# Optimization experiments

Hardware: AMD Instinct MI355X
Metric: run time of the kernel (lower is better)

Reference implementation:

```python
import jax, jax.numpy as jnp
import numpy as np


def setup_inputs() -> dict:
    key = jax.random.key(0)
    k1, k2 = jax.random.split(key)
    B, C, H, W, T = 8, 256, 64, 64, 512
    F_s = jax.random.normal(k1, (B, C, H, W), dtype=jnp.float32)
    F_t = jax.random.normal(k2, (B, T, C), dtype=jnp.float32)
    return {"F_s": F_s, "F_t": F_t}


def reference(F_s, F_t):
    B, C, H, W = F_s.shape
    T = F_t.shape[1]
    # [B, HW, C] spatial tokens
    F_s_t = jnp.transpose(F_s, (0, 2, 3, 1)).reshape(B, H * W, C)
    # scores [B, HW, T], scaled by sqrt(T) (softmax over last axis)
    A = jnp.einsum('bnc,btc->bnt', F_s_t, F_t) / jnp.sqrt(jnp.float32(T))
    A = jax.nn.softmax(A, axis=-1)
    # A^T @ F_s_t -> updated text tokens [B, T, C]
    F_t_updated = jnp.einsum('bnt,bnc->btc', A, F_s_t)
    # A @ F_t -> spatial update [B, HW, C]
    F_s_t_update = jnp.einsum('bnt,btc->bnc', A, F_t)
    F_s_t_update = jnp.transpose(F_s_t_update.reshape(B, H, W, C), (0, 3, 1, 2))
    F_s_updated = F_s + F_s_t_update
    return (F_s_updated, F_t_updated)
```

## Files before the change

kernel.cpp:

```cpp
#include <hip/hip_runtime.h>
#include <hip/hip_bf16.h>
#include <stdint.h>


typedef __attribute__((ext_vector_type(8))) short short8v;
typedef __attribute__((ext_vector_type(4))) float float4v;

#define MFMA16(a, b, c) __builtin_amdgcn_mfma_f32_16x16x32_bf16(a, b, c, 0, 0, 0)
#define SCALE 0.04419417382415922f

static __device__ __forceinline__ unsigned short f2bf(float f) {
  union { float f; uint32_t u; } v; v.f = f;
  uint32_t r = v.u + 0x7fffu + ((v.u >> 16) & 1u);
  return (unsigned short)(r >> 16);
}
static __device__ __forceinline__ float bf2f(unsigned short u) {
  union { uint32_t u; float f; } v; v.u = (uint32_t)u << 16;
  return v.f;
}

static __device__ __forceinline__ void gload16(const void* g, void* l) {
  __builtin_amdgcn_global_load_lds(
      (const __attribute__((address_space(1))) void*)g,
      (__attribute__((address_space(3))) void*)l, 16, 0, 0);
}

__global__ __launch_bounds__(256) void k_cast_transpose(
    const float* __restrict__ src, unsigned short* __restrict__ dstC,
    unsigned short* __restrict__ dstT, int R, int Cd) {
  __shared__ unsigned short tile[32][33];
  const size_t zoff = (size_t)blockIdx.z * R * Cd;
  const float* s = src + zoff;
  unsigned short* dc = dstC + zoff;
  unsigned short* dt = dstT + zoff;
  const int c0 = blockIdx.x * 32, r0 = blockIdx.y * 32;
  const int tid = threadIdx.x;
  const int r = tid >> 3, c4 = (tid & 7) * 4;

  float4 v = *(const float4*)&s[(size_t)(r0 + r) * Cd + c0 + c4];
  ushort4 bq;
  bq.x = f2bf(v.x); bq.y = f2bf(v.y); bq.z = f2bf(v.z); bq.w = f2bf(v.w);
  *(ushort4*)&dc[(size_t)(r0 + r) * Cd + c0 + c4] = bq;
  tile[r][c4 + 0] = bq.x; tile[r][c4 + 1] = bq.y;
  tile[r][c4 + 2] = bq.z; tile[r][c4 + 3] = bq.w;
  __syncthreads();
  ushort4 o;
  o.x = tile[c4 + 0][r]; o.y = tile[c4 + 1][r];
  o.z = tile[c4 + 2][r]; o.w = tile[c4 + 3][r];
  *(ushort4*)&dt[(size_t)(c0 + r) * R + r0 + c4] = o;
}

__global__ __launch_bounds__(256, 2) void k_attn(
    const unsigned short* __restrict__ Qg, const unsigned short* __restrict__ Kg,
    const unsigned short* __restrict__ VTg, const unsigned short* __restrict__ QTg,
    float* __restrict__ out0, unsigned short* __restrict__ PTg) {
  __shared__ char smem[81920];

  const int tid = threadIdx.x;
  const int wave = tid >> 6, lane = tid & 63;
  const int l16 = lane & 15, lhi = lane >> 4;
  const int b = blockIdx.x & 7, nb = blockIdx.x >> 3;
  const int n0w = nb * 64 + wave * 16;
  const int cx = (l16 & 7) << 4;

  const unsigned short* Qb = Qg + (size_t)b * 4096 * 256;
  const char* Kb = (const char*)(Kg + (size_t)b * 512 * 256);
  const char* VTb = (const char*)(VTg + (size_t)b * 256 * 512);

#define STAGE_K8(e_, buf_) do {                                             \
    const char* src_ = Kb + (e_) * 32768;                                   \
    _Pragma("unroll")                                                       \
    for (int i = 0; i < 8; i++) {                                           \
      const int off = (tid + i * 256) * 16;                                 \
      gload16(src_ + (off ^ (((off >> 9) & 7) << 4)),                       \
              smem + (buf_) * 32768 + off);                                 \
    } } while (0)

#define STAGE_VT(t_, buf_) do {                                             \
    _Pragma("unroll")                                                       \
    for (int i = 0; i < 8; i++) {                                           \
      const int off = (tid + i * 256) * 16;                                 \
      const int r_ = off >> 7, ic_ = off & 127;                             \
      gload16(VTb + (size_t)r_ * 1024 + (t_) * 128 + (ic_ ^ ((r_ & 7) << 4)), \
              smem + (buf_) * 32768 + off);                                 \
    } } while (0)

  short8v aQ[8];
#pragma unroll
  for (int kc = 0; kc < 8; kc++)
    aQ[kc] = *(const short8v*)(Qb + (size_t)(n0w + l16) * 256 + kc * 32 + lhi * 8);

  float4v acc[32];
#pragma unroll
  for (int tt = 0; tt < 32; tt++) acc[tt] = (float4v)0.f;

  STAGE_K8(0, 0);
  __syncthreads();
#pragma unroll
  for (int e = 0; e < 8; e++) {
    const int buf = e & 1;
    if (e < 7) STAGE_K8(e + 1, buf ^ 1);
    else       STAGE_VT(0, 0);
#pragma unroll
    for (int ti = 0; ti < 4; ti++) {
      const int row = ti * 16 + l16;
      const char* rb = smem + buf * 32768 + row * 512;
#pragma unroll
      for (int kc = 0; kc < 8; kc++) {
        short8v bf = *(const short8v*)(rb + ((kc * 64 + lhi * 16) ^ cx));
        acc[e * 4 + ti] = MFMA16(aQ[kc], bf, acc[e * 4 + ti]);
      }
    }
    if (e < 7) __syncthreads();
  }

  float mx[4], sm[4];
#pragma unroll
  for (int r = 0; r < 4; r++) {
    float m = acc[0][r];
#pragma unroll
    for (int tt = 1; tt < 32; tt++) m = fmaxf(m, acc[tt][r]);
    m = fmaxf(m, __shfl_xor(m, 1));
    m = fmaxf(m, __shfl_xor(m, 2));
    m = fmaxf(m, __shfl_xor(m, 4));
    m = fmaxf(m, __shfl_xor(m, 8));
    mx[r] = m;
  }
#pragma unroll
  for (int r = 0; r < 4; r++) {
    float s = 0.f;
#pragma unroll
    for (int tt = 0; tt < 32; tt++) {
      float p = __expf((acc[tt][r] - mx[r]) * SCALE);
      acc[tt][r] = p;
      s += p;
    }
    s += __shfl_xor(s, 1); s += __shfl_xor(s, 2);
    s += __shfl_xor(s, 4); s += __shfl_xor(s, 8);
    sm[r] = 1.0f / s;
  }

  uint32_t pk[64];
#pragma unroll
  for (int tt = 0; tt < 32; tt++)
#pragma unroll
    for (int h = 0; h < 2; h++)
      pk[tt * 2 + h] = (uint32_t)f2bf(acc[tt][2 * h] * sm[2 * h]) |
                       ((uint32_t)f2bf(acc[tt][2 * h + 1] * sm[2 * h + 1]) << 16);

  float4v oacc[16];
#pragma unroll
  for (int ct = 0; ct < 16; ct++) oacc[ct] = (float4v)0.f;

  unsigned short* PTb = PTg + (size_t)b * 512 * 4096;

#pragma unroll
  for (int tau = 0; tau < 8; tau++) {
    const int buf = tau & 1;
    __syncthreads();
    if (tau < 7) STAGE_VT(tau + 1, buf ^ 1);

    char* Psb = smem + 65536 + buf * 8192 + wave * 2048;
#pragma unroll
    for (int s = 0; s < 4; s++)
#pragma unroll
      for (int r = 0; r < 4; r++) {
        const int q = lhi * 4 + r, t2 = s * 16 + l16;
        const uint32_t w = pk[(tau * 4 + s) * 2 + (r >> 1)];
        *(unsigned short*)(Psb + ((q * 128 + t2 * 2) ^ ((q & 7) << 4))) =
            (unsigned short)(w >> ((r & 1) * 16));
      }

    short8v pb0 = *(const short8v*)(Psb + ((l16 * 128 + lhi * 16) ^ cx));
    short8v pb1 = *(const short8v*)(Psb + ((l16 * 128 + 64 + lhi * 16) ^ cx));
#pragma unroll
    for (int ct = 0; ct < 16; ct++) {
      const int row = ct * 16 + l16;
      const char* rb = smem + buf * 32768 + row * 128;
      short8v a0 = *(const short8v*)(rb + ((lhi * 16) ^ cx));
      oacc[ct] = MFMA16(a0, pb0, oacc[ct]);
      short8v a1 = *(const short8v*)(rb + ((64 + lhi * 16) ^ cx));
      oacc[ct] = MFMA16(a1, pb1, oacc[ct]);
    }

    {
      const int t2 = lane;
      unsigned short tmp[16];
#pragma unroll
      for (int q = 0; q < 16; q++)
        tmp[q] = *(const unsigned short*)(Psb + ((q * 128 + t2 * 2) ^ ((q & 7) << 4)));
      *(int4*)(PTb + (size_t)(tau * 64 + t2) * 4096 + n0w) = *(int4*)&tmp[0];
      *(int4*)(PTb + (size_t)(tau * 64 + t2) * 4096 + n0w + 8) = *(int4*)&tmp[8];
    }
  }

  const unsigned short* QTb = QTg + (size_t)b * 256 * 4096;
  float* o0 = out0 + (size_t)b * 256 * 4096;
#pragma unroll
  for (int ct = 0; ct < 16; ct++)
#pragma unroll
    for (int r = 0; r < 4; r++) {
      const int cgl = ct * 16 + lhi * 4 + r;
      const size_t off = (size_t)cgl * 4096 + n0w + l16;
      o0[off] = oacc[ct][r] + bf2f(QTb[off]);
    }
#undef STAGE_K8
#undef STAGE_VT
}

__global__ __launch_bounds__(256, 2) void k_ptq(
    const unsigned short* __restrict__ PTg, const unsigned short* __restrict__ QTg,
    float* __restrict__ part) {
  __shared__ char smem[65536];

  const int tid = threadIdx.x;
  const int wave = tid >> 6, lane = tid & 63;
  const int l16 = lane & 15, lhi = lane >> 4;
  const int bid = blockIdx.x;
  const int t0 = (bid >> 6) * 64;
  const int grp = bid & 63;
  const int b = grp & 7, ksl = grp >> 3;
  const int cx = (l16 & 7) << 4;

  const unsigned short* PTrow =
      PTg + ((size_t)(b * 512 + t0 + wave * 16 + l16)) * 4096 + ksl * 512 + lhi * 8;
  const char* QTb = (const char*)(QTg + (size_t)b * 256 * 4096 + ksl * 512);

#define STAGE_Q(c_, buf_) do {                                              \
    _Pragma("unroll")                                                       \
    for (int i = 0; i < 8; i++) {                                           \
      const int off = (tid + i * 256) * 16;                                 \
      const int r_ = off >> 7, ic_ = off & 127;                             \
      gload16(QTb + (size_t)r_ * 8192 + (c_) * 128 + (ic_ ^ ((r_ & 7) << 4)), \
              smem + (buf_) * 32768 + off);                                 \
    } } while (0)

  float4v acc[16];
#pragma unroll
  for (int ct = 0; ct < 16; ct++) acc[ct] = (float4v)0.f;

  STAGE_Q(0, 0);
  __syncthreads();
#pragma unroll
  for (int c = 0; c < 8; c++) {
    const int buf = c & 1;
    short8v pa0 = *(const short8v*)(PTrow + c * 64);
    short8v pa1 = *(const short8v*)(PTrow + c * 64 + 32);
    if (c < 7) STAGE_Q(c + 1, buf ^ 1);
#pragma unroll
    for (int ct = 0; ct < 16; ct++) {
      const int row = ct * 16 + l16;
      const char* rb = smem + buf * 32768 + row * 128;
      short8v b0 = *(const short8v*)(rb + ((lhi * 16) ^ cx));
      acc[ct] = MFMA16(pa0, b0, acc[ct]);
      short8v b1 = *(const short8v*)(rb + ((64 + lhi * 16) ^ cx));
      acc[ct] = MFMA16(pa1, b1, acc[ct]);
    }
    __syncthreads();
  }

  float* pout = part + (((size_t)ksl * 8 + b) * 512 + t0 + wave * 16) * 256;
#pragma unroll
  for (int ct = 0; ct < 16; ct++)
#pragma unroll
    for (int r = 0; r < 4; r++)
      pout[(lhi * 4 + r) * 256 + ct * 16 + l16] = acc[ct][r];
#undef STAGE_Q
}

__global__ __launch_bounds__(256) void k_red(
    const float* __restrict__ part, float* __restrict__ out1) {
  const int g = blockIdx.x * 256 + threadIdx.x;
  float4 s = *(const float4*)(part + (size_t)g * 4);
#pragma unroll
  for (int ksl = 1; ksl < 8; ksl++) {
    float4 v = *(const float4*)(part + (size_t)ksl * 1048576 + (size_t)g * 4);
    s.x += v.x; s.y += v.y; s.z += v.z; s.w += v.w;
  }
  *(float4*)(out1 + (size_t)g * 4) = s;
}

extern "C" void kernel_launch(void* const* d_in, const int* in_sizes, int n_in,
                              void* d_out, int out_size, void* d_ws, size_t ws_size,
                              hipStream_t stream) {
  const float* Fs = (const float*)d_in[0];
  const float* Ft = (const float*)d_in[1];
  float* out0 = (float*)d_out;
  float* out1 = out0 + (size_t)8 * 256 * 4096;

  unsigned short* ws = (unsigned short*)d_ws;
  unsigned short* Q  = ws;
  unsigned short* QT = Q + 8388608;
  unsigned short* K  = QT + 8388608;
  unsigned short* VT = K + 1048576;
  unsigned short* PT = VT + 1048576;
  float* part = (float*)(PT + 16777216);

  k_cast_transpose<<<dim3(128, 8, 8), 256, 0, stream>>>(Fs, QT, Q, 256, 4096);
  k_cast_transpose<<<dim3(8, 16, 8), 256, 0, stream>>>(Ft, K, VT, 512, 256);
  k_attn<<<dim3(512), 256, 0, stream>>>(Q, K, VT, QT, out0, PT);
  k_ptq<<<dim3(512), 256, 0, stream>>>(PT, QT, part);
  k_red<<<dim3(1024), 256, 0, stream>>>(part, out1);
}
```

Baseline: 83.08 us.

## Deepen k_attn staging to 4-buffer 16KB chunks and replace split-K reduce with atomics

The K and V^T staging in k_attn moves from two 32KB buffers to four 16KB buffers with three chunks in flight. Explicit vmcnt waits with raw s_barrier replace __syncthreads, so global-to-LDS loads overlap MFMA work more deeply. The separate partial-sum buffer and k_red reduction kernel are removed: k_ptq atomically adds its split-K partials into a zeroed out1. This saves a kernel launch and the partial write/read traffic, at the cost of scalar float atomics and non-deterministic summation order.

```diff
diff --git a/kernel.cpp b/kernel.cpp
--- a/kernel.cpp
+++ b/kernel.cpp
@@ -67,22 +67,25 @@
   const char* Kb = (const char*)(Kg + (size_t)b * 512 * 256);
   const char* VTb = (const char*)(VTg + (size_t)b * 256 * 512);
 
-#define STAGE_K8(e_, buf_) do {                                             \
-    const char* src_ = Kb + (e_) * 32768;                                   \
+#define STAGE_K16(c_) do {                                                  \
+    const char* src_ = Kb + (c_) * 16384;                                   \
+    char* dst_ = smem + ((c_) & 3) * 16384;                                 \
     _Pragma("unroll")                                                       \
-    for (int i = 0; i < 8; i++) {                                           \
+    for (int i = 0; i < 4; i++) {                                           \
       const int off = (tid + i * 256) * 16;                                 \
-      gload16(src_ + (off ^ (((off >> 9) & 7) << 4)),                       \
-              smem + (buf_) * 32768 + off);                                 \
+      gload16(src_ + (off ^ (((off >> 9) & 7) << 4)), dst_ + off);          \
     } } while (0)
 
-#define STAGE_VT(t_, buf_) do {                                             \
+#define STAGE_VT16(v_) do {                                                 \
+    const int ch_ = (v_) & 1, tau_ = (v_) >> 1;                             \
+    char* dst_ = smem + ((v_) & 3) * 16384;                                 \
     _Pragma("unroll")                                                       \
-    for (int i = 0; i < 8; i++) {                                           \
+    for (int i = 0; i < 4; i++) {                                           \
       const int off = (tid + i * 256) * 16;                                 \
       const int r_ = off >> 7, ic_ = off & 127;                             \
-      gload16(VTb + (size_t)r_ * 1024 + (t_) * 128 + (ic_ ^ ((r_ & 7) << 4)), \
-              smem + (buf_) * 32768 + off);                                 \
+      gload16(VTb + (size_t)(ch_ * 128 + r_) * 1024 + tau_ * 128            \
+                  + (ic_ ^ ((r_ & 7) << 4)),                                \
+              dst_ + off);                                                  \
     } } while (0)
 
   short8v aQ[8];
@@ -94,24 +97,24 @@
 #pragma unroll
   for (int tt = 0; tt < 32; tt++) acc[tt] = (float4v)0.f;
 
-  STAGE_K8(0, 0);
-  __syncthreads();
-#pragma unroll
-  for (int e = 0; e < 8; e++) {
-    const int buf = e & 1;
-    if (e < 7) STAGE_K8(e + 1, buf ^ 1);
-    else       STAGE_VT(0, 0);
-#pragma unroll
-    for (int ti = 0; ti < 4; ti++) {
-      const int row = ti * 16 + l16;
-      const char* rb = smem + buf * 32768 + row * 512;
+  STAGE_K16(0); STAGE_K16(1); STAGE_K16(2);
+#pragma unroll
+  for (int c = 0; c < 16; c++) {
+    asm volatile("s_waitcnt vmcnt(8)" ::: "memory");
+    __builtin_amdgcn_s_barrier();
+    if (c < 13) STAGE_K16(c + 3);
+    else        STAGE_VT16(c - 13);
+    const char* bufp = smem + (c & 3) * 16384;
+#pragma unroll
+    for (int ti = 0; ti < 2; ti++) {
+      const char* rb = bufp + (ti * 16 + l16) * 512;
 #pragma unroll
       for (int kc = 0; kc < 8; kc++) {
         short8v bf = *(const short8v*)(rb + ((kc * 64 + lhi * 16) ^ cx));
-        acc[e * 4 + ti] = MFMA16(aQ[kc], bf, acc[e * 4 + ti]);
+        acc[c * 2 + ti] = MFMA16(aQ[kc], bf, acc[c * 2 + ti]);
       }
     }
-    if (e < 7) __syncthreads();
+    asm volatile("s_waitcnt lgkmcnt(0)" ::: "memory");
   }
 
   float mx[4], sm[4];
@@ -153,37 +156,40 @@
   for (int ct = 0; ct < 16; ct++) oacc[ct] = (float4v)0.f;
 
   unsigned short* PTb = PTg + (size_t)b * 512 * 4096;
-
-#pragma unroll
-  for (int tau = 0; tau < 8; tau++) {
-    const int buf = tau & 1;
-    __syncthreads();
-    if (tau < 7) STAGE_VT(tau + 1, buf ^ 1);
-
-    char* Psb = smem + 65536 + buf * 8192 + wave * 2048;
-#pragma unroll
-    for (int s = 0; s < 4; s++)
-#pragma unroll
-      for (int r = 0; r < 4; r++) {
-        const int q = lhi * 4 + r, t2 = s * 16 + l16;
-        const uint32_t w = pk[(tau * 4 + s) * 2 + (r >> 1)];
-        *(unsigned short*)(Psb + ((q * 128 + t2 * 2) ^ ((q & 7) << 4))) =
-            (unsigned short)(w >> ((r & 1) * 16));
-      }
-
-    short8v pb0 = *(const short8v*)(Psb + ((l16 * 128 + lhi * 16) ^ cx));
-    short8v pb1 = *(const short8v*)(Psb + ((l16 * 128 + 64 + lhi * 16) ^ cx));
-#pragma unroll
-    for (int ct = 0; ct < 16; ct++) {
-      const int row = ct * 16 + l16;
-      const char* rb = smem + buf * 32768 + row * 128;
+  short8v pb0 = short8v{}, pb1 = short8v{};
+
+#pragma unroll
+  for (int v = 0; v < 16; v++) {
+    if (v <= 13)      asm volatile("s_waitcnt vmcnt(8)" ::: "memory");
+    else if (v == 14) asm volatile("s_waitcnt vmcnt(4)" ::: "memory");
+    else              asm volatile("s_waitcnt vmcnt(0)" ::: "memory");
+    __builtin_amdgcn_s_barrier();
+    if (v < 13) STAGE_VT16(v + 3);
+    const int tau = v >> 1, ch = v & 1;
+    char* Psb = smem + 65536 + (tau & 1) * 8192 + wave * 2048;
+    if (ch == 0) {
+#pragma unroll
+      for (int s = 0; s < 4; s++)
+#pragma unroll
+        for (int r = 0; r < 4; r++) {
+          const int q = lhi * 4 + r, t2 = s * 16 + l16;
+          const uint32_t w = pk[(tau * 4 + s) * 2 + (r >> 1)];
+          *(unsigned short*)(Psb + ((q * 128 + t2 * 2) ^ ((q & 7) << 4))) =
+              (unsigned short)(w >> ((r & 1) * 16));
+        }
+      pb0 = *(const short8v*)(Psb + ((l16 * 128 + lhi * 16) ^ cx));
+      pb1 = *(const short8v*)(Psb + ((l16 * 128 + 64 + lhi * 16) ^ cx));
+    }
+    const char* bufp = smem + (v & 3) * 16384;
+#pragma unroll
+    for (int ctl = 0; ctl < 8; ctl++) {
+      const char* rb = bufp + (ctl * 16 + l16) * 128;
       short8v a0 = *(const short8v*)(rb + ((lhi * 16) ^ cx));
-      oacc[ct] = MFMA16(a0, pb0, oacc[ct]);
+      oacc[ch * 8 + ctl] = MFMA16(a0, pb0, oacc[ch * 8 + ctl]);
       short8v a1 = *(const short8v*)(rb + ((64 + lhi * 16) ^ cx));
-      oacc[ct] = MFMA16(a1, pb1, oacc[ct]);
-    }
-
-    {
+      oacc[ch * 8 + ctl] = MFMA16(a1, pb1, oacc[ch * 8 + ctl]);
+    }
+    if (ch == 1) {
       const int t2 = lane;
       unsigned short tmp[16];
 #pragma unroll
@@ -192,6 +198,7 @@
       *(int4*)(PTb + (size_t)(tau * 64 + t2) * 4096 + n0w) = *(int4*)&tmp[0];
       *(int4*)(PTb + (size_t)(tau * 64 + t2) * 4096 + n0w + 8) = *(int4*)&tmp[8];
     }
+    asm volatile("s_waitcnt lgkmcnt(0)" ::: "memory");
   }
 
   const unsigned short* QTb = QTg + (size_t)b * 256 * 4096;
@@ -204,13 +211,13 @@
       const size_t off = (size_t)cgl * 4096 + n0w + l16;
       o0[off] = oacc[ct][r] + bf2f(QTb[off]);
     }
-#undef STAGE_K8
-#undef STAGE_VT
+#undef STAGE_K16
+#undef STAGE_VT16
 }
 
 __global__ __launch_bounds__(256, 2) void k_ptq(
     const unsigned short* __restrict__ PTg, const unsigned short* __restrict__ QTg,
-    float* __restrict__ part) {
+    float* __restrict__ out1) {
   __shared__ char smem[65536];
 
   const int tid = threadIdx.x;
@@ -259,25 +266,15 @@
     __syncthreads();
   }
 
-  float* pout = part + (((size_t)ksl * 8 + b) * 512 + t0 + wave * 16) * 256;
 #pragma unroll
   for (int ct = 0; ct < 16; ct++)
 #pragma unroll
-    for (int r = 0; r < 4; r++)
-      pout[(lhi * 4 + r) * 256 + ct * 16 + l16] = acc[ct][r];
+    for (int r = 0; r < 4; r++) {
+      const int t = t0 + wave * 16 + lhi * 4 + r;
+      const int cc = ct * 16 + l16;
+      atomicAdd(&out1[((size_t)b * 512 + t) * 256 + cc], acc[ct][r]);
+    }
 #undef STAGE_Q
-}
-
-__global__ __launch_bounds__(256) void k_red(
-    const float* __restrict__ part, float* __restrict__ out1) {
-  const int g = blockIdx.x * 256 + threadIdx.x;
-  float4 s = *(const float4*)(part + (size_t)g * 4);
-#pragma unroll
-  for (int ksl = 1; ksl < 8; ksl++) {
-    float4 v = *(const float4*)(part + (size_t)ksl * 1048576 + (size_t)g * 4);
-    s.x += v.x; s.y += v.y; s.z += v.z; s.w += v.w;
-  }
-  *(float4*)(out1 + (size_t)g * 4) = s;
 }
 
 extern "C" void kernel_launch(void* const* d_in, const int* in_sizes, int n_in,
@@ -294,11 +291,10 @@
   unsigned short* K  = QT + 8388608;
   unsigned short* VT = K + 1048576;
   unsigned short* PT = VT + 1048576;
-  float* part = (float*)(PT + 16777216);
-
+
+  hipMemsetAsync(out1, 0, (size_t)1048576 * sizeof(float), stream);
   k_cast_transpose<<<dim3(128, 8, 8), 256, 0, stream>>>(Fs, QT, Q, 256, 4096);
   k_cast_transpose<<<dim3(8, 16, 8), 256, 0, stream>>>(Ft, K, VT, 512, 256);
   k_attn<<<dim3(512), 256, 0, stream>>>(Q, K, VT, QT, out0, PT);
-  k_ptq<<<dim3(512), 256, 0, stream>>>(PT, QT, part);
-  k_red<<<dim3(1024), 256, 0, stream>>>(part, out1);
-}
+  k_ptq<<<dim3(512), 256, 0, stream>>>(PT, QT, out1);
+}
```

Result: slower. 99.81 us (+20.1%).
